# Kernel optimization log

Hardware: AMD Instinct MI355X
Metric: run time of the kernel (lower is better)

The kernel has to match this reference:

```python
import jax, jax.numpy as jnp
import numpy as np

INVALID_CLS = tuple(range(240, 256))
TEMPERATURE = 1.0
PRED_PER_IM = 100
B, Q, C = 256, 900, 256


def setup_inputs() -> dict:
    key = jax.random.key(0)
    k1, k2, k3, k4 = jax.random.split(key, 4)
    pred_logits = jax.random.normal(k1, (B, Q, C), dtype=jnp.float32)
    pred_obj = jax.random.uniform(k2, (B, Q), dtype=jnp.float32)
    pred_boxes = jax.random.uniform(k3, (B, Q, 4), dtype=jnp.float32)
    # target sizes ~ realistic image resolutions (h, w)
    target_sizes = jax.random.uniform(k4, (B, 2), dtype=jnp.float32) * 800.0 + 200.0
    return {"pred_logits": pred_logits, "pred_obj": pred_obj,
            "pred_boxes": pred_boxes, "target_sizes": target_sizes}


def _cxcywh_to_xyxy(boxes):
    cx, cy, w, h = jnp.split(boxes, 4, axis=-1)
    return jnp.concatenate([cx - 0.5 * w, cy - 0.5 * h,
                            cx + 0.5 * w, cy + 0.5 * h], axis=-1)


def reference(pred_logits, pred_obj, pred_boxes, target_sizes):
    b, q, c = pred_logits.shape
    invalid = jnp.array(INVALID_CLS)
    logits = pred_logits.at[:, :, invalid].set(-1e11)
    # fused probability: exp(-T * energy) * sigmoid(logits)
    obj_prob = jnp.exp(-TEMPERATURE * pred_obj)[..., None]          # [B,Q,1]
    fused = obj_prob * jax.nn.sigmoid(logits)                       # [B,Q,C]
    scores, topk_idx = jax.lax.top_k(fused.reshape(b, q * c), PRED_PER_IM)
    topk_boxes = topk_idx // c                                      # [B,K]
    labels = topk_idx % c                                           # [B,K]
    boxes_xyxy = _cxcywh_to_xyxy(pred_boxes)                        # [B,Q,4]
    gather_idx = jnp.broadcast_to(topk_boxes[:, :, None], (b, PRED_PER_IM, 4))
    boxes = jnp.take_along_axis(boxes_xyxy, gather_idx, axis=1)     # [B,K,4]
    img_h, img_w = target_sizes[:, 0], target_sizes[:, 1]
    scale = jnp.stack([img_w, img_h, img_w, img_h], axis=1)         # [B,4]
    boxes = boxes * scale[:, None, :]
    return scores, labels, boxes
```

## Files before the change

kernel.cpp:

```cpp
#include <hip/hip_runtime.h>
#include <stdint.h>

#define NB 256
#define NQ 900
#define NC 256
#define TOPK 100
#define QC (NQ * NC)
#define NBINS_S 4096
#define CAP 4096
#define FCAP 512
#define KS 25
#define SHIFT 18
#define MARGIN 4096u


__device__ __forceinline__ float fastsig(float x) {
    return __builtin_amdgcn_rcpf(1.0f + __expf(-x));
}

__global__ __launch_bounds__(1024)
void postproc_kernel(const float* __restrict__ logits,
                     const float* __restrict__ obj,
                     const float* __restrict__ pboxes,
                     const float* __restrict__ tsz,
                     float* __restrict__ out)
{
    const int b = blockIdx.x;
    const int tid = threadIdx.x;
    const int wid = tid >> 6;
    const int lane = tid & 63;

    __shared__ unsigned int pool[NBINS_S];
    __shared__ float eobj[NQ];
    __shared__ unsigned int cbits[CAP];
    __shared__ int cidx[CAP];
    __shared__ int activeQ[NQ];
    __shared__ unsigned int part[1024];
    __shared__ unsigned int part2[32];
    __shared__ int s_thrBin, s_cnt, s_nActive, s_c2;
    __shared__ int s_dig, s_above, s_nfin;

    unsigned int* shist = pool;

    for (int i = tid; i < NBINS_S; i += 1024) shist[i] = 0;
    if (tid == 0) { s_cnt = 0; s_nActive = 0; }
    if (tid < NQ) eobj[tid] = expf(-obj[b * NQ + tid]);
    __syncthreads();

    const float4* lg4 = (const float4*)(logits + (size_t)b * QC);

    for (int j = wid; j < 56; j += 16) {
        int q = j * 16 + 8;
        if (lane < 60) {
            float eo = eobj[q];
            float4 v = lg4[(q << 6) + lane];
            atomicAdd(&shist[__float_as_uint(eo * fastsig(v.x)) >> SHIFT], 1u);
            atomicAdd(&shist[__float_as_uint(eo * fastsig(v.y)) >> SHIFT], 1u);
            atomicAdd(&shist[__float_as_uint(eo * fastsig(v.z)) >> SHIFT], 1u);
            atomicAdd(&shist[__float_as_uint(eo * fastsig(v.w)) >> SHIFT], 1u);
        }
    }
    __syncthreads();

    {
        unsigned int sum = 0;
        #pragma unroll
        for (int j = 0; j < 4; ++j) sum += shist[tid * 4 + j];
        part[tid] = sum;
    }
    __syncthreads();
    if (tid < 32) {
        unsigned int s2 = 0;
        #pragma unroll
        for (int j = 0; j < 32; ++j) s2 += part[tid * 32 + j];
        part2[tid] = s2;
    }
    __syncthreads();
    if (tid == 0) {
        int cum = 0;
        int sc = 31;
        while (sc > 0 && cum + (int)part2[sc] < KS) { cum += (int)part2[sc]; --sc; }
        int pc = sc * 32 + 31, plo = sc * 32;
        while (pc > plo && cum + (int)part[pc] < KS) { cum += (int)part[pc]; --pc; }
        int bin = pc * 4 + 3, blo = pc * 4;
        while (bin > blo && cum + (int)shist[bin] < KS) { cum += (int)shist[bin]; --bin; }
        s_thrBin = bin;
    }
    __syncthreads();
    unsigned int thrBits = (unsigned int)s_thrBin << SHIFT;

    if (tid < NQ) {
        if (__float_as_uint(eobj[tid]) >= thrBits) {
            int p = atomicAdd(&s_nActive, 1);
            activeQ[p] = tid;
        }
    }
    __syncthreads();
    const int nA = s_nActive;

    const unsigned preThr = (thrBits > MARGIN) ? (thrBits - MARGIN) : 0u;
    for (int j = wid; j < nA; j += 16) {
        int q = activeQ[j];
        if (lane < 60) {
            float eo = eobj[q];
            float4 v = lg4[(q << 6) + lane];
            #pragma unroll
            for (int j2 = 0; j2 < 4; ++j2) {
                float x = (j2 == 0) ? v.x : (j2 == 1) ? v.y : (j2 == 2) ? v.z : v.w;
                unsigned fb = __float_as_uint(eo * fastsig(x));
                if (fb >= preThr) {
                    int p = atomicAdd(&s_cnt, 1);
                    if (p < CAP) {
                        cbits[p] = __float_as_uint(x);
                        cidx[p] = (q << 8) + (lane << 2) + j2;
                    }
                }
            }
        }
    }
    __syncthreads();
    const int npreRaw = s_cnt;
    const int npre = min(npreRaw, CAP);

    int myN = 0;
    int midx0 = 0, midx1 = 0, midx2 = 0, midx3 = 0;
    float mlog0 = 0.f, mlog1 = 0.f, mlog2 = 0.f, mlog3 = 0.f;
    {
        int i = tid;
        if (i < npre) { midx0 = cidx[i]; mlog0 = __uint_as_float(cbits[i]); myN = 1; i += 1024; }
        if (i < npre) { midx1 = cidx[i]; mlog1 = __uint_as_float(cbits[i]); myN = 2; i += 1024; }
        if (i < npre) { midx2 = cidx[i]; mlog2 = __uint_as_float(cbits[i]); myN = 3; i += 1024; }
        if (i < npre) { midx3 = cidx[i]; mlog3 = __uint_as_float(cbits[i]); myN = 4; }
    }
    __syncthreads();
    if (tid == 0) s_cnt = 0;
    __syncthreads();

    #pragma unroll
    for (int k = 0; k < 4; ++k) {
        if (k < myN) {
            float x  = (k == 0) ? mlog0 : (k == 1) ? mlog1 : (k == 2) ? mlog2 : mlog3;
            int  idx = (k == 0) ? midx0 : (k == 1) ? midx1 : (k == 2) ? midx2 : midx3;
            float eo = eobj[idx >> 8];
            float s = eo * (1.0f / (1.0f + expf(-x)));
            unsigned bits = __float_as_uint(s);
            if (bits >= thrBits) {
                int p = atomicAdd(&s_cnt, 1);
                if (p < CAP) { cbits[p] = bits; cidx[p] = idx; }
            }
        }
    }
    __syncthreads();
    int M = s_cnt;

    if (M < TOPK || npreRaw > CAP) {
        int lo = 0, hi = NBINS_S - 1;
        while (lo < hi) {
            int mid = (lo + hi + 1) >> 1;
            unsigned int tb = (unsigned int)mid << SHIFT;
            if (tid == 0) s_c2 = 0;
            __syncthreads();
            int local = 0;
            for (int j = wid; j < NQ; j += 16) {
                if (__float_as_uint(eobj[j]) >= tb && lane < 60) {
                    float eo = eobj[j];
                    float4 v = lg4[(j << 6) + lane];
                    local += (__float_as_uint(eo * (1.0f / (1.0f + expf(-v.x)))) >= tb);
                    local += (__float_as_uint(eo * (1.0f / (1.0f + expf(-v.y)))) >= tb);
                    local += (__float_as_uint(eo * (1.0f / (1.0f + expf(-v.z)))) >= tb);
                    local += (__float_as_uint(eo * (1.0f / (1.0f + expf(-v.w)))) >= tb);
                }
            }
            atomicAdd(&s_c2, local);
            __syncthreads();
            if (s_c2 >= TOPK) lo = mid; else hi = mid - 1;
            __syncthreads();
        }
        unsigned int tb = (unsigned int)lo << SHIFT;
        thrBits = tb;
        if (tid == 0) s_cnt = 0;
        __syncthreads();
        for (int j = wid; j < NQ; j += 16) {
            if (__float_as_uint(eobj[j]) >= tb && lane < 60) {
                float eo = eobj[j];
                float4 v = lg4[(j << 6) + lane];
                #pragma unroll
                for (int j2 = 0; j2 < 4; ++j2) {
                    float x = (j2 == 0) ? v.x : (j2 == 1) ? v.y : (j2 == 2) ? v.z : v.w;
                    float s = eo * (1.0f / (1.0f + expf(-x)));
                    unsigned int bits = __float_as_uint(s);
                    if (bits >= tb) {
                        int p = atomicAdd(&s_cnt, 1);
                        if (p < CAP) {
                            cbits[p] = bits;
                            cidx[p] = (j << 8) + (lane << 2) + j2;
                        }
                    }
                }
            }
        }
        __syncthreads();
        M = s_cnt;
    }
    M = min(M, CAP);

    unsigned int* rhist = part;
    unsigned int* rsuf  = part + 256;
    unsigned int prefixVal = 0;
    int need = TOPK;
    int startShift = 24;
    if ((thrBits >> 24) == 0x3Fu) { prefixVal = 0x3F000000u; startShift = 16; }
    for (int shift = startShift; shift >= 0; shift -= 8) {
        if (tid < 256) rhist[tid] = 0;
        __syncthreads();
        unsigned int pmask = (shift >= 24) ? 0u : (0xFFFFFFFFu << (shift + 8));
        for (int i = tid; i < M; i += 1024) {
            unsigned int bb = cbits[i];
            if ((bb & pmask) == (prefixVal & pmask))
                atomicAdd(&rhist[(bb >> shift) & 255], 1u);
        }
        __syncthreads();
        if (tid < 64) {
            unsigned int h0 = rhist[tid * 4 + 0];
            unsigned int h1 = rhist[tid * 4 + 1];
            unsigned int h2 = rhist[tid * 4 + 2];
            unsigned int h3 = rhist[tid * 4 + 3];
            unsigned int loc = h0 + h1 + h2 + h3;
            unsigned int suf = loc;
            #pragma unroll
            for (int d = 1; d < 64; d <<= 1) {
                unsigned int o = __shfl_down(suf, d);
                suf += (tid + d < 64) ? o : 0u;
            }
            unsigned int above = suf - loc;
            rsuf[tid * 4 + 3] = above + h3;
            rsuf[tid * 4 + 2] = above + h3 + h2;
            rsuf[tid * 4 + 1] = above + h3 + h2 + h1;
            rsuf[tid * 4 + 0] = above + h3 + h2 + h1 + h0;
        }
        __syncthreads();
        if (tid < 256) {
            int sv = (int)rsuf[tid];
            int sa = (tid == 255) ? 0 : (int)rsuf[tid + 1];
            if (sv >= need && sa < need) { s_dig = tid; s_above = sa; }
        }
        __syncthreads();
        prefixVal |= ((unsigned int)s_dig) << shift;
        need -= s_above;
    }
    const unsigned int kth = prefixVal;

    unsigned int* fb = pool;
    int* fi = (int*)(pool + FCAP);
    if (tid == 0) s_nfin = 0;
    __syncthreads();
    for (int i = tid; i < M; i += 1024) {
        unsigned int bb = cbits[i];
        if (bb >= kth) {
            int p = atomicAdd(&s_nfin, 1);
            if (p < FCAP) { fb[p] = bb; fi[p] = cidx[i]; }
        }
    }
    __syncthreads();
    const int n = min(s_nfin, FCAP);

    const float ih = tsz[b * 2 + 0];
    const float iw = tsz[b * 2 + 1];
    float* out_scores = out;
    float* out_labels = out + NB * TOPK;
    float* out_boxes  = out + 2 * NB * TOPK;

    for (int i = tid; i < n; i += 1024) {
        unsigned int mb = fb[i];
        int mi = fi[i];
        int rank = 0;
        for (int j = 0; j < n; ++j) {
            unsigned int ob = fb[j];
            int oi = fi[j];
            rank += (ob > mb) || (ob == mb && oi < mi);
        }
        if (rank < TOPK) {
            int q = mi >> 8;
            int c = mi & 255;
            out_scores[b * TOPK + rank] = __uint_as_float(mb);
            out_labels[b * TOPK + rank] = (float)c;
            const float* bp = pboxes + ((size_t)b * NQ + q) * 4;
            float cx = bp[0], cy = bp[1], w = bp[2], h = bp[3];
            float* dst = out_boxes + ((size_t)b * TOPK + rank) * 4;
            dst[0] = (cx - 0.5f * w) * iw;
            dst[1] = (cy - 0.5f * h) * ih;
            dst[2] = (cx + 0.5f * w) * iw;
            dst[3] = (cy + 0.5f * h) * ih;
        }
    }
}

extern "C" void kernel_launch(void* const* d_in, const int* in_sizes, int n_in,
                              void* d_out, int out_size, void* d_ws, size_t ws_size,
                              hipStream_t stream) {
    const float* logits = (const float*)d_in[0];
    const float* obj    = (const float*)d_in[1];
    const float* boxes  = (const float*)d_in[2];
    const float* tsz    = (const float*)d_in[3];
    float* out = (float*)d_out;
    hipLaunchKernelGGL(postproc_kernel, dim3(NB), dim3(1024), 0, stream,
                       logits, obj, boxes, tsz, out);
}
```

Before: 34.05 us.

## Run radix select and final ranking in a single wavefront without block barriers

Moves the radix-select refinement, final candidate compaction and rank-based output stage onto wave 0 alone. Block-wide __syncthreads are replaced by wave barriers, digit selection uses a ballot/shuffle in registers, and compaction uses ballot prefix counts instead of shared atomics. This removes many block-level barriers and shared-memory atomics in the tail, at the cost of doing the candidate scans and the O(n^2) rank loop with only 64 threads.

```diff
diff --git a/kernel.cpp b/kernel.cpp
--- a/kernel.cpp
+++ b/kernel.cpp
@@ -38,7 +38,6 @@
     __shared__ unsigned int part[1024];
     __shared__ unsigned int part2[32];
     __shared__ int s_thrBin, s_cnt, s_nActive, s_c2;
-    __shared__ int s_dig, s_above, s_nfin;
 
     unsigned int* shist = pool;
 
@@ -204,93 +203,100 @@
     }
     M = min(M, CAP);
 
-    unsigned int* rhist = part;
-    unsigned int* rsuf  = part + 256;
-    unsigned int prefixVal = 0;
-    int need = TOPK;
-    int startShift = 24;
-    if ((thrBits >> 24) == 0x3Fu) { prefixVal = 0x3F000000u; startShift = 16; }
-    for (int shift = startShift; shift >= 0; shift -= 8) {
-        if (tid < 256) rhist[tid] = 0;
-        __syncthreads();
-        unsigned int pmask = (shift >= 24) ? 0u : (0xFFFFFFFFu << (shift + 8));
-        for (int i = tid; i < M; i += 1024) {
-            unsigned int bb = cbits[i];
-            if ((bb & pmask) == (prefixVal & pmask))
-                atomicAdd(&rhist[(bb >> shift) & 255], 1u);
-        }
-        __syncthreads();
-        if (tid < 64) {
-            unsigned int h0 = rhist[tid * 4 + 0];
-            unsigned int h1 = rhist[tid * 4 + 1];
-            unsigned int h2 = rhist[tid * 4 + 2];
-            unsigned int h3 = rhist[tid * 4 + 3];
-            unsigned int loc = h0 + h1 + h2 + h3;
-            unsigned int suf = loc;
+    if (wid == 0) {
+        unsigned* rh = part;
+
+        unsigned prefixVal = 0;
+        int need = TOPK;
+        int startShift = 24;
+        if ((thrBits >> 24) == 0x3Fu) { prefixVal = 0x3F000000u; startShift = 16; }
+        for (int shift = startShift; shift >= 0; shift -= 8) {
+            rh[lane] = 0; rh[lane + 256 - 192] = 0;
+            rh[lane + 128] = 0; rh[lane + 192] = 0;
+            __builtin_amdgcn_wave_barrier();
+            unsigned pmask = (shift >= 24) ? 0u : (0xFFFFFFFFu << (shift + 8));
+            for (int i = lane; i < M; i += 64) {
+                unsigned bb = cbits[i];
+                if ((bb & pmask) == (prefixVal & pmask))
+                    atomicAdd(&rh[(bb >> shift) & 255], 1u);
+            }
+            __builtin_amdgcn_wave_barrier();
+            __threadfence_block();
+            unsigned h0 = rh[lane * 4 + 0];
+            unsigned h1 = rh[lane * 4 + 1];
+            unsigned h2 = rh[lane * 4 + 2];
+            unsigned h3 = rh[lane * 4 + 3];
+            unsigned loc = h0 + h1 + h2 + h3;
+            unsigned suf = loc;
             #pragma unroll
             for (int d = 1; d < 64; d <<= 1) {
-                unsigned int o = __shfl_down(suf, d);
-                suf += (tid + d < 64) ? o : 0u;
-            }
-            unsigned int above = suf - loc;
-            rsuf[tid * 4 + 3] = above + h3;
-            rsuf[tid * 4 + 2] = above + h3 + h2;
-            rsuf[tid * 4 + 1] = above + h3 + h2 + h1;
-            rsuf[tid * 4 + 0] = above + h3 + h2 + h1 + h0;
-        }
-        __syncthreads();
-        if (tid < 256) {
-            int sv = (int)rsuf[tid];
-            int sa = (tid == 255) ? 0 : (int)rsuf[tid + 1];
-            if (sv >= need && sa < need) { s_dig = tid; s_above = sa; }
-        }
-        __syncthreads();
-        prefixVal |= ((unsigned int)s_dig) << shift;
-        need -= s_above;
-    }
-    const unsigned int kth = prefixVal;
-
-    unsigned int* fb = pool;
-    int* fi = (int*)(pool + FCAP);
-    if (tid == 0) s_nfin = 0;
-    __syncthreads();
-    for (int i = tid; i < M; i += 1024) {
-        unsigned int bb = cbits[i];
-        if (bb >= kth) {
-            int p = atomicAdd(&s_nfin, 1);
-            if (p < FCAP) { fb[p] = bb; fi[p] = cidx[i]; }
-        }
-    }
-    __syncthreads();
-    const int n = min(s_nfin, FCAP);
-
-    const float ih = tsz[b * 2 + 0];
-    const float iw = tsz[b * 2 + 1];
-    float* out_scores = out;
-    float* out_labels = out + NB * TOPK;
-    float* out_boxes  = out + 2 * NB * TOPK;
-
-    for (int i = tid; i < n; i += 1024) {
-        unsigned int mb = fb[i];
-        int mi = fi[i];
-        int rank = 0;
-        for (int j = 0; j < n; ++j) {
-            unsigned int ob = fb[j];
-            int oi = fi[j];
-            rank += (ob > mb) || (ob == mb && oi < mi);
-        }
-        if (rank < TOPK) {
-            int q = mi >> 8;
-            int c = mi & 255;
-            out_scores[b * TOPK + rank] = __uint_as_float(mb);
-            out_labels[b * TOPK + rank] = (float)c;
-            const float* bp = pboxes + ((size_t)b * NQ + q) * 4;
-            float cx = bp[0], cy = bp[1], w = bp[2], h = bp[3];
-            float* dst = out_boxes + ((size_t)b * TOPK + rank) * 4;
-            dst[0] = (cx - 0.5f * w) * iw;
-            dst[1] = (cy - 0.5f * h) * ih;
-            dst[2] = (cx + 0.5f * w) * iw;
-            dst[3] = (cy + 0.5f * h) * ih;
+                unsigned o = __shfl_down(suf, d);
+                if (lane + d < 64) suf += o;
+            }
+            int nb = (int)(suf - loc);
+            int c3 = nb + (int)h3;
+            int c2 = c3 + (int)h2;
+            int c1 = c2 + (int)h1;
+            int c0 = c1 + (int)h0;
+            int dig = -1, abv = 0;
+            if      (c3 >= need && nb < need) { dig = 4 * lane + 3; abv = nb; }
+            else if (c2 >= need && c3 < need) { dig = 4 * lane + 2; abv = c3; }
+            else if (c1 >= need && c2 < need) { dig = 4 * lane + 1; abv = c2; }
+            else if (c0 >= need && c1 < need) { dig = 4 * lane + 0; abv = c1; }
+            unsigned long long bm = __ballot(dig >= 0);
+            int src = __ffsll((unsigned long long)bm) - 1;
+            dig = __shfl(dig, src);
+            abv = __shfl(abv, src);
+            prefixVal |= ((unsigned)dig) << shift;
+            need -= abv;
+        }
+        const unsigned kth = prefixVal;
+
+        unsigned* fbw = pool;
+        int* fiw = (int*)(pool + FCAP);
+        const int Mpad = (M + 63) & ~63;
+        int nf = 0;
+        for (int i = lane; i < Mpad; i += 64) {
+            bool p = (i < M) && (cbits[i] >= kth);
+            unsigned long long m = __ballot(p);
+            if (p) {
+                int pos = nf + __popcll(m & ((1ull << lane) - 1ull));
+                if (pos < FCAP) { fbw[pos] = cbits[i]; fiw[pos] = cidx[i]; }
+            }
+            nf += __popcll(m);
+        }
+        const int n = min(nf, FCAP);
+        __builtin_amdgcn_wave_barrier();
+        __threadfence_block();
+
+        const float ih = tsz[b * 2 + 0];
+        const float iw = tsz[b * 2 + 1];
+        float* out_scores = out;
+        float* out_labels = out + NB * TOPK;
+        float* out_boxes  = out + 2 * NB * TOPK;
+
+        for (int i = lane; i < n; i += 64) {
+            unsigned mb = fbw[i];
+            int mi = fiw[i];
+            int rank = 0;
+            for (int j = 0; j < n; ++j) {
+                unsigned ob = fbw[j];
+                int oi = fiw[j];
+                rank += (ob > mb) || (ob == mb && oi < mi);
+            }
+            if (rank < TOPK) {
+                int q = mi >> 8;
+                int c = mi & 255;
+                out_scores[b * TOPK + rank] = __uint_as_float(mb);
+                out_labels[b * TOPK + rank] = (float)c;
+                const float* bp = pboxes + ((size_t)b * NQ + q) * 4;
+                float cx = bp[0], cy = bp[1], w = bp[2], h = bp[3];
+                float* dst = out_boxes + ((size_t)b * TOPK + rank) * 4;
+                dst[0] = (cx - 0.5f * w) * iw;
+                dst[1] = (cy - 0.5f * h) * ih;
+                dst[2] = (cx + 0.5f * w) * iw;
+                dst[3] = (cy + 0.5f * h) * ih;
+            }
         }
     }
 }
```

Measured after the change: 52.87 us. 1.55x slower.
